# Optimization experiments

Measured on AMD Instinct MI355X. Metric: run time of the kernel, lower is better.

Reference implementation:

```python
import jax, jax.numpy as jnp
import numpy as np

N, E, F_IN, H, G, C = 50000, 800000, 128, 128, 64, 10
EPS = 1e-5


def _glorot_lin(key, fin, fout):
    s = 1.0 / np.sqrt(fin)
    return jax.random.uniform(key, (fin, fout), jnp.float32, -s, s)


def setup_inputs() -> dict:
    key = jax.random.key(0)
    ks = jax.random.split(key, 24)
    x = jax.random.normal(ks[0], (N, F_IN), jnp.float32)
    edge_index = jax.random.randint(ks[1], (2, E), 0, N)
    batch = jnp.sort(jax.random.randint(ks[2], (N,), 0, G))
    inp = {"x": x, "edge_index": edge_index, "batch": batch}
    # GCNConv weights [in, out] and biases
    dims = [(F_IN, H), (H, H), (H, H), (H, H)]
    for i, (fi, fo) in enumerate(dims, start=1):
        inp[f"W{i}"] = _glorot_lin(ks[2 + i], fi, fo)
        inp[f"b{i}"] = jnp.zeros((fo,), jnp.float32)
    # BatchNorm affine params
    for i in range(1, 4):
        inp[f"g{i}"] = jnp.ones((H,), jnp.float32)
        inp[f"be{i}"] = jnp.zeros((H,), jnp.float32)
    # MLP head
    inp["lw1"] = _glorot_lin(ks[10], 2 * H, H)
    inp["lb1"] = jnp.zeros((H,), jnp.float32)
    inp["lw2"] = _glorot_lin(ks[11], H, C)
    inp["lb2"] = jnp.zeros((C,), jnp.float32)
    return inp


def _gcn_conv(h_in, W, b, src, dst, norm_e, self_norm):
    # linear transform then symmetric-normalized aggregation (incl. self loops)
    h = h_in @ W                                            # [N, out]
    agg = jax.ops.segment_sum(h[src] * norm_e[:, None], dst, num_segments=N)
    return agg + h * self_norm[:, None] + b


def _batch_norm(x, gamma, beta):
    mu = jnp.mean(x, axis=0)
    var = jnp.var(x, axis=0)
    return (x - mu) * jax.lax.rsqrt(var + EPS) * gamma + beta


def reference(x, edge_index, batch, W1, b1, W2, b2, W3, b3, W4, b4,
              g1, be1, g2, be2, g3, be3, lw1, lb1, lw2, lb2):
    src, dst = edge_index[0], edge_index[1]
    # degrees with self loops; GCN symmetric normalization
    deg = jax.ops.segment_sum(jnp.ones((E,), jnp.float32), dst, num_segments=N) + 1.0
    dinv = jax.lax.rsqrt(deg)
    norm_e = dinv[src] * dinv[dst]   # per-edge norm
    self_norm = 1.0 / deg            # self-loop norm = dinv*dinv

    h = jax.nn.relu(_batch_norm(_gcn_conv(x, W1, b1, src, dst, norm_e, self_norm), g1, be1))
    h = jax.nn.relu(_batch_norm(_gcn_conv(h, W2, b2, src, dst, norm_e, self_norm), g2, be2))
    h = jax.nn.relu(_batch_norm(_gcn_conv(h, W3, b3, src, dst, norm_e, self_norm), g3, be3))
    h = jax.nn.relu(_gcn_conv(h, W4, b4, src, dst, norm_e, self_norm))

    counts = jax.ops.segment_sum(jnp.ones((N,), jnp.float32), batch, num_segments=G)
    x_mean = jax.ops.segment_sum(h, batch, num_segments=G) / counts[:, None]
    x_max = jax.ops.segment_max(h, batch, num_segments=G)
    z = jnp.concatenate([x_mean, x_max], axis=1)            # [G, 2H]

    z = jax.nn.relu(z @ lw1 + lb1)
    # dropout is identity in eval mode
    return z @ lw2 + lb2                                    # [G, C]
```

## Files before the change

kernel.cpp:

```cpp
#include <hip/hip_runtime.h>

#define N_NODES 50000
#define N_EDGES 800000
#define HID     128
#define NGRAPH  64
#define BN_EPS  1e-5f
#define SCAN_B  98

__global__ __launch_bounds__(256) void degbounds_kernel(const int* __restrict__ ei,
                                                        int* __restrict__ degi,
                                                        const int* __restrict__ batch,
                                                        int* __restrict__ bound) {
    const int i = blockIdx.x * 256 + threadIdx.x;
    if (i < N_EDGES) atomicAdd(&degi[ei[N_EDGES + i]], 1);
    if (i < N_NODES) {
        const int b = batch[i];
        if (i == 0) {
            for (int g = 0; g <= b; ++g) bound[g] = 0;
        } else {
            const int pb = batch[i - 1];
            for (int g = pb + 1; g <= b; ++g) bound[g] = i;
        }
        if (i == N_NODES - 1) {
            for (int g = b + 1; g <= NGRAPH; ++g) bound[g] = N_NODES;
        }
    }
}

__global__ __launch_bounds__(512) void scan1_kernel(const int* __restrict__ degi,
                                                    int* __restrict__ row_start,
                                                    int* __restrict__ partials,
                                                    float* __restrict__ dinv) {
    __shared__ int sh[512];
    const int t = threadIdx.x;
    const int i = blockIdx.x * 512 + t;
    const int v = (i < N_NODES) ? degi[i] : 0;
    if (i < N_NODES) dinv[i] = rsqrtf((float)v + 1.0f);
    sh[t] = v;
    __syncthreads();
#pragma unroll
    for (int off = 1; off < 512; off <<= 1) {
        const int add = (t >= off) ? sh[t - off] : 0;
        __syncthreads();
        sh[t] += add;
        __syncthreads();
    }
    if (i < N_NODES) row_start[i] = sh[t] - v;
    if (t == 511) partials[blockIdx.x] = sh[511];
}

__global__ __launch_bounds__(128) void scan2_kernel(int* __restrict__ partials,
                                                    int* __restrict__ row_start) {
    __shared__ int sh[SCAN_B + 1];
    const int t = threadIdx.x;
    if (t < SCAN_B) sh[t] = partials[t];
    __syncthreads();
    if (t == 0) {
        int run = 0;
        for (int b = 0; b < SCAN_B; ++b) { const int v = sh[b]; sh[b] = run; run += v; }
        sh[SCAN_B] = run;
    }
    __syncthreads();
    if (t < SCAN_B) partials[t] = sh[t];
    if (t == 0) row_start[N_NODES] = sh[SCAN_B];
}

__global__ __launch_bounds__(512) void scan3_kernel(int* __restrict__ row_start,
                                                    const int* __restrict__ partials) {
    const int i = blockIdx.x * 512 + threadIdx.x;
    if (i < N_NODES) row_start[i] += partials[blockIdx.x];
}

__global__ __launch_bounds__(256) void scatter_kernel(const int* __restrict__ ei,
                                                      const float* __restrict__ dinv,
                                                      const int* __restrict__ row_start,
                                                      int* __restrict__ cursor,
                                                      float2* __restrict__ csr_sw) {
    int e = blockIdx.x * 256 + threadIdx.x;
    if (e >= N_EDGES) return;
    const int src = ei[e];
    const int dst = ei[N_EDGES + e];
    const int pos = row_start[dst] + atomicAdd(&cursor[dst], 1);
    float2 sw;
    sw.x = __int_as_float(src);
    sw.y = dinv[src] * dinv[dst];
    csr_sw[pos] = sw;
}

__global__ __launch_bounds__(256) void gemm_kernel(const float* __restrict__ X,
                                                   const float* __restrict__ W,
                                                   const float* __restrict__ stats,
                                                   const float* __restrict__ gamma,
                                                   const float* __restrict__ beta,
                                                   const int use_bn,
                                                   float* __restrict__ hout) {
    __shared__ float xs[64][128];
    __shared__ float wsm[32][128];
    __shared__ float scs[128], shs[128];
    const int tid = threadIdx.x;
    const int block_row = blockIdx.x * 64;

    if (use_bn && tid < 128) {
        const float invN = 1.0f / (float)N_NODES;
        const float mu = stats[tid] * invN;
        const float var = stats[128 + tid] * invN - mu * mu;
        const float sc = rsqrtf(var + BN_EPS) * gamma[tid];
        scs[tid] = sc;
        shs[tid] = fmaf(-mu, sc, beta[tid]);
    }
    if (use_bn) __syncthreads();

    {
        const float4* Xv = (const float4*)(X + (size_t)block_row * HID);
        float4* xsv = (float4*)&xs[0][0];
        int rows_valid = N_NODES - block_row;
        if (rows_valid > 64) rows_valid = 64;
        const int max4 = rows_valid * 32;
        for (int i = tid; i < 64 * 32; i += 256) {
            float4 v = (i < max4) ? Xv[i] : make_float4(0.f, 0.f, 0.f, 0.f);
            if (use_bn) {
                const int c4 = (i & 31) * 4;
                const float4 sc = *(const float4*)&scs[c4];
                const float4 sh = *(const float4*)&shs[c4];
                v.x = fmaxf(fmaf(v.x, sc.x, sh.x), 0.f);
                v.y = fmaxf(fmaf(v.y, sc.y, sh.y), 0.f);
                v.z = fmaxf(fmaf(v.z, sc.z, sh.z), 0.f);
                v.w = fmaxf(fmaf(v.w, sc.w, sh.w), 0.f);
            }
            xsv[i] = v;
        }
    }

    const int cg = (tid & 31) * 4;
    const int r0 = (tid >> 5) * 8;

    float acc[8][4];
#pragma unroll
    for (int r = 0; r < 8; ++r)
#pragma unroll
        for (int j = 0; j < 4; ++j) acc[r][j] = 0.f;

    for (int kc = 0; kc < 4; ++kc) {
        __syncthreads();
        {
            const float4* Wv = (const float4*)(W + kc * 32 * HID);
            float4* wsv = (float4*)&wsm[0][0];
            for (int i = tid; i < 32 * 32; i += 256) wsv[i] = Wv[i];
        }
        __syncthreads();
#pragma unroll
        for (int kk = 0; kk < 32; ++kk) {
            const float4 w4 = *(const float4*)(&wsm[kk][cg]);
            const int k = kc * 32 + kk;
#pragma unroll
            for (int r = 0; r < 8; ++r) {
                const float xv = xs[r0 + r][k];
                acc[r][0] = fmaf(xv, w4.x, acc[r][0]);
                acc[r][1] = fmaf(xv, w4.y, acc[r][1]);
                acc[r][2] = fmaf(xv, w4.z, acc[r][2]);
                acc[r][3] = fmaf(xv, w4.w, acc[r][3]);
            }
        }
    }

#pragma unroll
    for (int r = 0; r < 8; ++r) {
        const int row = block_row + r0 + r;
        if (row < N_NODES)
            *(float4*)(hout + (size_t)row * HID + cg) =
                make_float4(acc[r][0], acc[r][1], acc[r][2], acc[r][3]);
    }
}

__global__ __launch_bounds__(256) void agg_csr_kernel(const int* __restrict__ row_start,
                                                      const float2* __restrict__ csr_sw,
                                                      const float* __restrict__ h,
                                                      const float* __restrict__ dinv,
                                                      const float* __restrict__ bias,
                                                      float* __restrict__ agg) {
    const int node = blockIdx.x * 4 + (threadIdx.x >> 6);
    if (node >= N_NODES) return;
    const int lane = threadIdx.x & 63;
    const int c = lane * 2;
    const int beg = row_start[node];
    const int end = row_start[node + 1];

    const float dv = dinv[node];
    const float sn = dv * dv;
    const float2 hv = *(const float2*)(h + (size_t)node * HID + c);
    const float2 bv = *(const float2*)(bias + c);
    float2 a0 = make_float2(fmaf(hv.x, sn, bv.x), fmaf(hv.y, sn, bv.y));
    float2 a1 = make_float2(0.f, 0.f), a2 = make_float2(0.f, 0.f),
           a3 = make_float2(0.f, 0.f), a4 = make_float2(0.f, 0.f),
           a5 = make_float2(0.f, 0.f), a6 = make_float2(0.f, 0.f),
           a7 = make_float2(0.f, 0.f);

    int p = beg;
    for (; p + 8 <= end; p += 8) {
        const float2 e0 = csr_sw[p];
        const float2 e1 = csr_sw[p + 1];
        const float2 e2 = csr_sw[p + 2];
        const float2 e3 = csr_sw[p + 3];
        const float2 e4 = csr_sw[p + 4];
        const float2 e5 = csr_sw[p + 5];
        const float2 e6 = csr_sw[p + 6];
        const float2 e7 = csr_sw[p + 7];
        const float2 v0 = *(const float2*)(h + (size_t)__float_as_int(e0.x) * HID + c);
        const float2 v1 = *(const float2*)(h + (size_t)__float_as_int(e1.x) * HID + c);
        const float2 v2 = *(const float2*)(h + (size_t)__float_as_int(e2.x) * HID + c);
        const float2 v3 = *(const float2*)(h + (size_t)__float_as_int(e3.x) * HID + c);
        const float2 v4 = *(const float2*)(h + (size_t)__float_as_int(e4.x) * HID + c);
        const float2 v5 = *(const float2*)(h + (size_t)__float_as_int(e5.x) * HID + c);
        const float2 v6 = *(const float2*)(h + (size_t)__float_as_int(e6.x) * HID + c);
        const float2 v7 = *(const float2*)(h + (size_t)__float_as_int(e7.x) * HID + c);
        a0.x = fmaf(v0.x, e0.y, a0.x); a0.y = fmaf(v0.y, e0.y, a0.y);
        a1.x = fmaf(v1.x, e1.y, a1.x); a1.y = fmaf(v1.y, e1.y, a1.y);
        a2.x = fmaf(v2.x, e2.y, a2.x); a2.y = fmaf(v2.y, e2.y, a2.y);
        a3.x = fmaf(v3.x, e3.y, a3.x); a3.y = fmaf(v3.y, e3.y, a3.y);
        a4.x = fmaf(v4.x, e4.y, a4.x); a4.y = fmaf(v4.y, e4.y, a4.y);
        a5.x = fmaf(v5.x, e5.y, a5.x); a5.y = fmaf(v5.y, e5.y, a5.y);
        a6.x = fmaf(v6.x, e6.y, a6.x); a6.y = fmaf(v6.y, e6.y, a6.y);
        a7.x = fmaf(v7.x, e7.y, a7.x); a7.y = fmaf(v7.y, e7.y, a7.y);
    }
    for (; p + 4 <= end; p += 4) {
        const float2 e0 = csr_sw[p];
        const float2 e1 = csr_sw[p + 1];
        const float2 e2 = csr_sw[p + 2];
        const float2 e3 = csr_sw[p + 3];
        const float2 v0 = *(const float2*)(h + (size_t)__float_as_int(e0.x) * HID + c);
        const float2 v1 = *(const float2*)(h + (size_t)__float_as_int(e1.x) * HID + c);
        const float2 v2 = *(const float2*)(h + (size_t)__float_as_int(e2.x) * HID + c);
        const float2 v3 = *(const float2*)(h + (size_t)__float_as_int(e3.x) * HID + c);
        a0.x = fmaf(v0.x, e0.y, a0.x); a0.y = fmaf(v0.y, e0.y, a0.y);
        a1.x = fmaf(v1.x, e1.y, a1.x); a1.y = fmaf(v1.y, e1.y, a1.y);
        a2.x = fmaf(v2.x, e2.y, a2.x); a2.y = fmaf(v2.y, e2.y, a2.y);
        a3.x = fmaf(v3.x, e3.y, a3.x); a3.y = fmaf(v3.y, e3.y, a3.y);
    }
    for (; p < end; ++p) {
        const float2 e0 = csr_sw[p];
        const float2 v0 = *(const float2*)(h + (size_t)__float_as_int(e0.x) * HID + c);
        a0.x = fmaf(v0.x, e0.y, a0.x); a0.y = fmaf(v0.y, e0.y, a0.y);
    }
    a0.x += (a1.x + a2.x) + (a3.x + a4.x) + (a5.x + a6.x) + a7.x;
    a0.y += (a1.y + a2.y) + (a3.y + a4.y) + (a5.y + a6.y) + a7.y;
    *(float2*)(agg + (size_t)node * HID + c) = a0;
}

__global__ __launch_bounds__(256) void bn_stats_kernel(const float* __restrict__ a,
                                                       float* __restrict__ stats) {
    const int c = threadIdx.x & 127;
    const int half = threadIdx.x >> 7;
    const int row0 = blockIdx.x * 128;
    int rend = row0 + 128;
    if (rend > N_NODES) rend = N_NODES;
    float s = 0.f, sq = 0.f;
    for (int r = row0 + half; r < rend; r += 2) {
        const float v = a[(size_t)r * HID + c];
        s += v;
        sq = fmaf(v, v, sq);
    }
    __shared__ float sh[2][2][128];
    sh[0][half][c] = s;
    sh[1][half][c] = sq;
    __syncthreads();
    if (half == 0) {
        atomicAdd(&stats[c], sh[0][0][c] + sh[0][1][c]);
        atomicAdd(&stats[HID + c], sh[1][0][c] + sh[1][1][c]);
    }
}

__global__ __launch_bounds__(256) void pool_seg_kernel(const float* __restrict__ a,
                                                       const int* __restrict__ bound,
                                                       float* __restrict__ z) {
    const int g = blockIdx.x;
    const int cl = threadIdx.x & 31;
    const int c = blockIdx.y * 32 + cl;
    const int par = threadIdx.x >> 5;
    const int beg = bound[g], end = bound[g + 1];
    float s = 0.f, m = 0.f;
    for (int r = beg + par; r < end; r += 8) {
        const float v = fmaxf(a[(size_t)r * HID + c], 0.f);
        s += v;
        m = fmaxf(m, v);
    }
    __shared__ float ssum[8][32];
    __shared__ float smax[8][32];
    ssum[par][cl] = s;
    smax[par][cl] = m;
    __syncthreads();
    if (par == 0) {
        float ts = 0.f, tm = 0.f;
#pragma unroll
        for (int p = 0; p < 8; ++p) { ts += ssum[p][cl]; tm = fmaxf(tm, smax[p][cl]); }
        const float cntf = (float)(end - beg);
        z[g * 256 + c] = ts / fmaxf(cntf, 1.f);
        z[g * 256 + 128 + c] = tm;
    }
}

__global__ __launch_bounds__(128) void head_kernel(const float* __restrict__ z,
                                                   const float* __restrict__ lw1,
                                                   const float* __restrict__ lb1,
                                                   const float* __restrict__ lw2,
                                                   const float* __restrict__ lb2,
                                                   float* __restrict__ out) {
    __shared__ float zin[256];
    __shared__ float z1[128];
    const int g = blockIdx.x;
    const int t = threadIdx.x;
    zin[t] = z[g * 256 + t];
    zin[128 + t] = z[g * 256 + 128 + t];
    __syncthreads();
    float accv = lb1[t];
#pragma unroll 4
    for (int k = 0; k < 256; ++k) accv = fmaf(zin[k], lw1[k * 128 + t], accv);
    z1[t] = fmaxf(accv, 0.f);
    __syncthreads();
    if (t < 10) {
        float o = lb2[t];
#pragma unroll 4
        for (int k = 0; k < 128; ++k) o = fmaf(z1[k], lw2[k * 10 + t], o);
        out[g * 10 + t] = o;
    }
}

extern "C" void kernel_launch(void* const* d_in, const int* in_sizes, int n_in,
                              void* d_out, int out_size, void* d_ws, size_t ws_size,
                              hipStream_t stream) {
    const float* x     = (const float*)d_in[0];
    const int*   ei    = (const int*)d_in[1];
    const int*   batch = (const int*)d_in[2];
    const float* W[4]  = {(const float*)d_in[3], (const float*)d_in[5],
                          (const float*)d_in[7], (const float*)d_in[9]};
    const float* B[4]  = {(const float*)d_in[4], (const float*)d_in[6],
                          (const float*)d_in[8], (const float*)d_in[10]};
    const float* Gm[3] = {(const float*)d_in[11], (const float*)d_in[13],
                          (const float*)d_in[15]};
    const float* Be[3] = {(const float*)d_in[12], (const float*)d_in[14],
                          (const float*)d_in[16]};
    const float* lw1 = (const float*)d_in[17];
    const float* lb1 = (const float*)d_in[18];
    const float* lw2 = (const float*)d_in[19];
    const float* lb2 = (const float*)d_in[20];

    char* ws = (char*)d_ws;
    float*  dinv      = (float*)ws;
    float*  stats     = (float*)(ws + 50000u * 4);
    float*  z         = (float*)(ws + 50256u * 4);
    int*    degi      = (int*)  (ws + 66640u * 4);
    int*    cursor    = (int*)  (ws + 116640u * 4);
    int*    row_start = (int*)  (ws + 166640u * 4);
    int*    bound     = (int*)  (ws + 216644u * 4);
    float2* csr_sw    = (float2*)(ws + 216712u * 4);
    float*  hbuf      = (float*)(ws + 1816712u * 4);
    float*  abuf      = (float*)(ws + 8216712u * 4);
    int*    partials  = (int*)  (ws + 14616712u * 4);

    hipMemsetAsync(degi, 0, 100000u * sizeof(int), stream);
    degbounds_kernel<<<(N_EDGES + 255) / 256, 256, 0, stream>>>(ei, degi, batch, bound);
    scan1_kernel<<<SCAN_B, 512, 0, stream>>>(degi, row_start, partials, dinv);
    scan2_kernel<<<1, 128, 0, stream>>>(partials, row_start);
    scan3_kernel<<<SCAN_B, 512, 0, stream>>>(row_start, partials);
    scatter_kernel<<<(N_EDGES + 255) / 256, 256, 0, stream>>>(ei, dinv, row_start,
                                                              cursor, csr_sw);

    const float* cur = x;
    for (int l = 0; l < 4; ++l) {
        gemm_kernel<<<(N_NODES + 63) / 64, 256, 0, stream>>>(
            cur, W[l], stats, l > 0 ? Gm[l - 1] : Gm[0], l > 0 ? Be[l - 1] : Be[0],
            l > 0 ? 1 : 0, hbuf);
        agg_csr_kernel<<<(N_NODES + 3) / 4, 256, 0, stream>>>(row_start, csr_sw, hbuf,
                                                              dinv, B[l], abuf);
        if (l < 3) {
            hipMemsetAsync(stats, 0, 256 * sizeof(float), stream);
            bn_stats_kernel<<<(N_NODES + 127) / 128, 256, 0, stream>>>(abuf, stats);
        }
        cur = abuf;
    }

    pool_seg_kernel<<<dim3(NGRAPH, 4), 256, 0, stream>>>(abuf, bound, z);
    head_kernel<<<NGRAPH, 128, 0, stream>>>(z, lw1, lb1, lw2, lb2, (float*)d_out);
}
```

Baseline: 742.8 us.

## Fuse BN statistics into CSR aggregation and retile GEMM with swizzled shared memory

The separate bn_stats kernel and its per-layer memset are removed. The aggregation kernel becomes a grid-stride loop over a fixed 2048-block grid that accumulates per-channel sum and sum-of-squares and atomically adds them into a per-layer stats slice, which is zeroed once up front. This avoids re-reading the 25.6 MB activation buffer three times and cuts launches. The GEMM is retiled to 4 rows by 8 columns per thread with an XOR-swizzled X tile and float4 X reads, reducing LDS bank conflicts and LDS traffic per FMA. The fixed grid may lower occupancy balance for the gather.

```diff
diff --git a/kernel.cpp b/kernel.cpp
--- a/kernel.cpp
+++ b/kernel.cpp
@@ -6,6 +6,7 @@
 #define NGRAPH  64
 #define BN_EPS  1e-5f
 #define SCAN_B  98
+#define AGG_GRID 2048
 
 __global__ __launch_bounds__(256) void degbounds_kernel(const int* __restrict__ ei,
                                                         int* __restrict__ degi,
@@ -111,15 +112,15 @@
     if (use_bn) __syncthreads();
 
     {
-        const float4* Xv = (const float4*)(X + (size_t)block_row * HID);
-        float4* xsv = (float4*)&xs[0][0];
         int rows_valid = N_NODES - block_row;
         if (rows_valid > 64) rows_valid = 64;
-        const int max4 = rows_valid * 32;
         for (int i = tid; i < 64 * 32; i += 256) {
-            float4 v = (i < max4) ? Xv[i] : make_float4(0.f, 0.f, 0.f, 0.f);
+            const int r = i >> 5;
+            const int c4 = (i & 31) * 4;
+            float4 v = make_float4(0.f, 0.f, 0.f, 0.f);
+            if (r < rows_valid)
+                v = *(const float4*)(X + (size_t)(block_row + r) * HID + c4);
             if (use_bn) {
-                const int c4 = (i & 31) * 4;
                 const float4 sc = *(const float4*)&scs[c4];
                 const float4 sh = *(const float4*)&shs[c4];
                 v.x = fmaxf(fmaf(v.x, sc.x, sh.x), 0.f);
@@ -127,18 +128,19 @@
                 v.z = fmaxf(fmaf(v.z, sc.z, sh.z), 0.f);
                 v.w = fmaxf(fmaf(v.w, sc.w, sh.w), 0.f);
             }
-            xsv[i] = v;
-        }
-    }
-
-    const int cg = (tid & 31) * 4;
-    const int r0 = (tid >> 5) * 8;
-
-    float acc[8][4];
-#pragma unroll
-    for (int r = 0; r < 8; ++r)
-#pragma unroll
-        for (int j = 0; j < 4; ++j) acc[r][j] = 0.f;
+            *(float4*)&xs[r][c4 ^ (((r >> 2) & 3) << 2)] = v;
+        }
+    }
+
+    const int cgA = (tid & 15) * 4;
+    const int r0 = (tid >> 4) * 4;
+    const int kswz = ((r0 >> 2) & 3) << 2;
+
+    float acc[4][8];
+#pragma unroll
+    for (int r = 0; r < 4; ++r)
+#pragma unroll
+        for (int j = 0; j < 8; ++j) acc[r][j] = 0.f;
 
     for (int kc = 0; kc < 4; ++kc) {
         __syncthreads();
@@ -149,26 +151,41 @@
         }
         __syncthreads();
 #pragma unroll
-        for (int kk = 0; kk < 32; ++kk) {
-            const float4 w4 = *(const float4*)(&wsm[kk][cg]);
-            const int k = kc * 32 + kk;
-#pragma unroll
-            for (int r = 0; r < 8; ++r) {
-                const float xv = xs[r0 + r][k];
-                acc[r][0] = fmaf(xv, w4.x, acc[r][0]);
-                acc[r][1] = fmaf(xv, w4.y, acc[r][1]);
-                acc[r][2] = fmaf(xv, w4.z, acc[r][2]);
-                acc[r][3] = fmaf(xv, w4.w, acc[r][3]);
+        for (int kk4 = 0; kk4 < 32; kk4 += 4) {
+            float4 xv[4];
+#pragma unroll
+            for (int j = 0; j < 4; ++j)
+                xv[j] = *(const float4*)&xs[r0 + j][(kc * 32 + kk4) ^ kswz];
+#pragma unroll
+            for (int dk = 0; dk < 4; ++dk) {
+                const float4 wa = *(const float4*)&wsm[kk4 + dk][cgA];
+                const float4 wb = *(const float4*)&wsm[kk4 + dk][cgA + 64];
+#pragma unroll
+                for (int r = 0; r < 4; ++r) {
+                    const float xvv = ((const float*)&xv[r])[dk];
+                    acc[r][0] = fmaf(xvv, wa.x, acc[r][0]);
+                    acc[r][1] = fmaf(xvv, wa.y, acc[r][1]);
+                    acc[r][2] = fmaf(xvv, wa.z, acc[r][2]);
+                    acc[r][3] = fmaf(xvv, wa.w, acc[r][3]);
+                    acc[r][4] = fmaf(xvv, wb.x, acc[r][4]);
+                    acc[r][5] = fmaf(xvv, wb.y, acc[r][5]);
+                    acc[r][6] = fmaf(xvv, wb.z, acc[r][6]);
+                    acc[r][7] = fmaf(xvv, wb.w, acc[r][7]);
+                }
             }
         }
     }
 
 #pragma unroll
-    for (int r = 0; r < 8; ++r) {
+    for (int r = 0; r < 4; ++r) {
         const int row = block_row + r0 + r;
-        if (row < N_NODES)
-            *(float4*)(hout + (size_t)row * HID + cg) =
+        if (row < N_NODES) {
+            float* hp = hout + (size_t)row * HID;
+            *(float4*)(hp + cgA) =
                 make_float4(acc[r][0], acc[r][1], acc[r][2], acc[r][3]);
+            *(float4*)(hp + cgA + 64) =
+                make_float4(acc[r][4], acc[r][5], acc[r][6], acc[r][7]);
+        }
     }
 }
 
@@ -177,95 +194,99 @@
                                                       const float* __restrict__ h,
                                                       const float* __restrict__ dinv,
                                                       const float* __restrict__ bias,
-                                                      float* __restrict__ agg) {
-    const int node = blockIdx.x * 4 + (threadIdx.x >> 6);
-    if (node >= N_NODES) return;
+                                                      float* __restrict__ agg,
+                                                      float* __restrict__ stats_out,
+                                                      const int do_stats) {
     const int lane = threadIdx.x & 63;
+    const int wv = threadIdx.x >> 6;
     const int c = lane * 2;
-    const int beg = row_start[node];
-    const int end = row_start[node + 1];
-
-    const float dv = dinv[node];
-    const float sn = dv * dv;
-    const float2 hv = *(const float2*)(h + (size_t)node * HID + c);
     const float2 bv = *(const float2*)(bias + c);
-    float2 a0 = make_float2(fmaf(hv.x, sn, bv.x), fmaf(hv.y, sn, bv.y));
-    float2 a1 = make_float2(0.f, 0.f), a2 = make_float2(0.f, 0.f),
-           a3 = make_float2(0.f, 0.f), a4 = make_float2(0.f, 0.f),
-           a5 = make_float2(0.f, 0.f), a6 = make_float2(0.f, 0.f),
-           a7 = make_float2(0.f, 0.f);
-
-    int p = beg;
-    for (; p + 8 <= end; p += 8) {
-        const float2 e0 = csr_sw[p];
-        const float2 e1 = csr_sw[p + 1];
-        const float2 e2 = csr_sw[p + 2];
-        const float2 e3 = csr_sw[p + 3];
-        const float2 e4 = csr_sw[p + 4];
-        const float2 e5 = csr_sw[p + 5];
-        const float2 e6 = csr_sw[p + 6];
-        const float2 e7 = csr_sw[p + 7];
-        const float2 v0 = *(const float2*)(h + (size_t)__float_as_int(e0.x) * HID + c);
-        const float2 v1 = *(const float2*)(h + (size_t)__float_as_int(e1.x) * HID + c);
-        const float2 v2 = *(const float2*)(h + (size_t)__float_as_int(e2.x) * HID + c);
-        const float2 v3 = *(const float2*)(h + (size_t)__float_as_int(e3.x) * HID + c);
-        const float2 v4 = *(const float2*)(h + (size_t)__float_as_int(e4.x) * HID + c);
-        const float2 v5 = *(const float2*)(h + (size_t)__float_as_int(e5.x) * HID + c);
-        const float2 v6 = *(const float2*)(h + (size_t)__float_as_int(e6.x) * HID + c);
-        const float2 v7 = *(const float2*)(h + (size_t)__float_as_int(e7.x) * HID + c);
-        a0.x = fmaf(v0.x, e0.y, a0.x); a0.y = fmaf(v0.y, e0.y, a0.y);
-        a1.x = fmaf(v1.x, e1.y, a1.x); a1.y = fmaf(v1.y, e1.y, a1.y);
-        a2.x = fmaf(v2.x, e2.y, a2.x); a2.y = fmaf(v2.y, e2.y, a2.y);
-        a3.x = fmaf(v3.x, e3.y, a3.x); a3.y = fmaf(v3.y, e3.y, a3.y);
-        a4.x = fmaf(v4.x, e4.y, a4.x); a4.y = fmaf(v4.y, e4.y, a4.y);
-        a5.x = fmaf(v5.x, e5.y, a5.x); a5.y = fmaf(v5.y, e5.y, a5.y);
-        a6.x = fmaf(v6.x, e6.y, a6.x); a6.y = fmaf(v6.y, e6.y, a6.y);
-        a7.x = fmaf(v7.x, e7.y, a7.x); a7.y = fmaf(v7.y, e7.y, a7.y);
-    }
-    for (; p + 4 <= end; p += 4) {
-        const float2 e0 = csr_sw[p];
-        const float2 e1 = csr_sw[p + 1];
-        const float2 e2 = csr_sw[p + 2];
-        const float2 e3 = csr_sw[p + 3];
-        const float2 v0 = *(const float2*)(h + (size_t)__float_as_int(e0.x) * HID + c);
-        const float2 v1 = *(const float2*)(h + (size_t)__float_as_int(e1.x) * HID + c);
-        const float2 v2 = *(const float2*)(h + (size_t)__float_as_int(e2.x) * HID + c);
-        const float2 v3 = *(const float2*)(h + (size_t)__float_as_int(e3.x) * HID + c);
-        a0.x = fmaf(v0.x, e0.y, a0.x); a0.y = fmaf(v0.y, e0.y, a0.y);
-        a1.x = fmaf(v1.x, e1.y, a1.x); a1.y = fmaf(v1.y, e1.y, a1.y);
-        a2.x = fmaf(v2.x, e2.y, a2.x); a2.y = fmaf(v2.y, e2.y, a2.y);
-        a3.x = fmaf(v3.x, e3.y, a3.x); a3.y = fmaf(v3.y, e3.y, a3.y);
-    }
-    for (; p < end; ++p) {
-        const float2 e0 = csr_sw[p];
-        const float2 v0 = *(const float2*)(h + (size_t)__float_as_int(e0.x) * HID + c);
-        a0.x = fmaf(v0.x, e0.y, a0.x); a0.y = fmaf(v0.y, e0.y, a0.y);
-    }
-    a0.x += (a1.x + a2.x) + (a3.x + a4.x) + (a5.x + a6.x) + a7.x;
-    a0.y += (a1.y + a2.y) + (a3.y + a4.y) + (a5.y + a6.y) + a7.y;
-    *(float2*)(agg + (size_t)node * HID + c) = a0;
-}
-
-__global__ __launch_bounds__(256) void bn_stats_kernel(const float* __restrict__ a,
-                                                       float* __restrict__ stats) {
-    const int c = threadIdx.x & 127;
-    const int half = threadIdx.x >> 7;
-    const int row0 = blockIdx.x * 128;
-    int rend = row0 + 128;
-    if (rend > N_NODES) rend = N_NODES;
-    float s = 0.f, sq = 0.f;
-    for (int r = row0 + half; r < rend; r += 2) {
-        const float v = a[(size_t)r * HID + c];
-        s += v;
-        sq = fmaf(v, v, sq);
-    }
-    __shared__ float sh[2][2][128];
-    sh[0][half][c] = s;
-    sh[1][half][c] = sq;
-    __syncthreads();
-    if (half == 0) {
-        atomicAdd(&stats[c], sh[0][0][c] + sh[0][1][c]);
-        atomicAdd(&stats[HID + c], sh[1][0][c] + sh[1][1][c]);
+
+    float2 ssum = make_float2(0.f, 0.f);
+    float2 ssq  = make_float2(0.f, 0.f);
+
+    for (int base = blockIdx.x * 4; base < N_NODES; base += AGG_GRID * 4) {
+        const int node = base + wv;
+        if (node >= N_NODES) continue;
+        const int beg = row_start[node];
+        const int end = row_start[node + 1];
+
+        const float dv = dinv[node];
+        const float sn = dv * dv;
+        const float2 hv = *(const float2*)(h + (size_t)node * HID + c);
+        float2 a0 = make_float2(fmaf(hv.x, sn, bv.x), fmaf(hv.y, sn, bv.y));
+        float2 a1 = make_float2(0.f, 0.f), a2 = make_float2(0.f, 0.f),
+               a3 = make_float2(0.f, 0.f), a4 = make_float2(0.f, 0.f),
+               a5 = make_float2(0.f, 0.f), a6 = make_float2(0.f, 0.f),
+               a7 = make_float2(0.f, 0.f);
+
+        int p = beg;
+        for (; p + 8 <= end; p += 8) {
+            const float2 e0 = csr_sw[p];
+            const float2 e1 = csr_sw[p + 1];
+            const float2 e2 = csr_sw[p + 2];
+            const float2 e3 = csr_sw[p + 3];
+            const float2 e4 = csr_sw[p + 4];
+            const float2 e5 = csr_sw[p + 5];
+            const float2 e6 = csr_sw[p + 6];
+            const float2 e7 = csr_sw[p + 7];
+            const float2 v0 = *(const float2*)(h + (size_t)__float_as_int(e0.x) * HID + c);
+            const float2 v1 = *(const float2*)(h + (size_t)__float_as_int(e1.x) * HID + c);
+            const float2 v2 = *(const float2*)(h + (size_t)__float_as_int(e2.x) * HID + c);
+            const float2 v3 = *(const float2*)(h + (size_t)__float_as_int(e3.x) * HID + c);
+            const float2 v4 = *(const float2*)(h + (size_t)__float_as_int(e4.x) * HID + c);
+            const float2 v5 = *(const float2*)(h + (size_t)__float_as_int(e5.x) * HID + c);
+            const float2 v6 = *(const float2*)(h + (size_t)__float_as_int(e6.x) * HID + c);
+            const float2 v7 = *(const float2*)(h + (size_t)__float_as_int(e7.x) * HID + c);
+            a0.x = fmaf(v0.x, e0.y, a0.x); a0.y = fmaf(v0.y, e0.y, a0.y);
+            a1.x = fmaf(v1.x, e1.y, a1.x); a1.y = fmaf(v1.y, e1.y, a1.y);
+            a2.x = fmaf(v2.x, e2.y, a2.x); a2.y = fmaf(v2.y, e2.y, a2.y);
+            a3.x = fmaf(v3.x, e3.y, a3.x); a3.y = fmaf(v3.y, e3.y, a3.y);
+            a4.x = fmaf(v4.x, e4.y, a4.x); a4.y = fmaf(v4.y, e4.y, a4.y);
+            a5.x = fmaf(v5.x, e5.y, a5.x); a5.y = fmaf(v5.y, e5.y, a5.y);
+            a6.x = fmaf(v6.x, e6.y, a6.x); a6.y = fmaf(v6.y, e6.y, a6.y);
+            a7.x = fmaf(v7.x, e7.y, a7.x); a7.y = fmaf(v7.y, e7.y, a7.y);
+        }
+        for (; p + 4 <= end; p += 4) {
+            const float2 e0 = csr_sw[p];
+            const float2 e1 = csr_sw[p + 1];
+            const float2 e2 = csr_sw[p + 2];
+            const float2 e3 = csr_sw[p + 3];
+            const float2 v0 = *(const float2*)(h + (size_t)__float_as_int(e0.x) * HID + c);
+            const float2 v1 = *(const float2*)(h + (size_t)__float_as_int(e1.x) * HID + c);
+            const float2 v2 = *(const float2*)(h + (size_t)__float_as_int(e2.x) * HID + c);
+            const float2 v3 = *(const float2*)(h + (size_t)__float_as_int(e3.x) * HID + c);
+            a0.x = fmaf(v0.x, e0.y, a0.x); a0.y = fmaf(v0.y, e0.y, a0.y);
+            a1.x = fmaf(v1.x, e1.y, a1.x); a1.y = fmaf(v1.y, e1.y, a1.y);
+            a2.x = fmaf(v2.x, e2.y, a2.x); a2.y = fmaf(v2.y, e2.y, a2.y);
+            a3.x = fmaf(v3.x, e3.y, a3.x); a3.y = fmaf(v3.y, e3.y, a3.y);
+        }
+        for (; p < end; ++p) {
+            const float2 e0 = csr_sw[p];
+            const float2 v0 = *(const float2*)(h + (size_t)__float_as_int(e0.x) * HID + c);
+            a0.x = fmaf(v0.x, e0.y, a0.x); a0.y = fmaf(v0.y, e0.y, a0.y);
+        }
+        a0.x += (a1.x + a2.x) + (a3.x + a4.x) + (a5.x + a6.x) + a7.x;
+        a0.y += (a1.y + a2.y) + (a3.y + a4.y) + (a5.y + a6.y) + a7.y;
+        *(float2*)(agg + (size_t)node * HID + c) = a0;
+
+        ssum.x += a0.x; ssum.y += a0.y;
+        ssq.x = fmaf(a0.x, a0.x, ssq.x); ssq.y = fmaf(a0.y, a0.y, ssq.y);
+    }
+
+    if (do_stats) {
+        __shared__ float s1[4][128];
+        __shared__ float s2[4][128];
+        s1[wv][c] = ssum.x; s1[wv][c + 1] = ssum.y;
+        s2[wv][c] = ssq.x;  s2[wv][c + 1] = ssq.y;
+        __syncthreads();
+        const int t = threadIdx.x;
+        if (t < 128) {
+            atomicAdd(&stats_out[t], s1[0][t] + s1[1][t] + s1[2][t] + s1[3][t]);
+        } else {
+            const int c2 = t - 128;
+            atomicAdd(&stats_out[128 + c2], s2[0][c2] + s2[1][c2] + s2[2][c2] + s2[3][c2]);
+        }
     }
 }
 
@@ -345,18 +366,19 @@
 
     char* ws = (char*)d_ws;
     float*  dinv      = (float*)ws;
-    float*  stats     = (float*)(ws + 50000u * 4);
-    float*  z         = (float*)(ws + 50256u * 4);
-    int*    degi      = (int*)  (ws + 66640u * 4);
-    int*    cursor    = (int*)  (ws + 116640u * 4);
-    int*    row_start = (int*)  (ws + 166640u * 4);
-    int*    bound     = (int*)  (ws + 216644u * 4);
-    float2* csr_sw    = (float2*)(ws + 216712u * 4);
-    float*  hbuf      = (float*)(ws + 1816712u * 4);
-    float*  abuf      = (float*)(ws + 8216712u * 4);
-    int*    partials  = (int*)  (ws + 14616712u * 4);
+    float*  stats3    = (float*)(ws + 50000u * 4);
+    float*  z         = (float*)(ws + 50768u * 4);
+    int*    degi      = (int*)  (ws + 67152u * 4);
+    int*    cursor    = (int*)  (ws + 117152u * 4);
+    int*    row_start = (int*)  (ws + 167152u * 4);
+    int*    bound     = (int*)  (ws + 217156u * 4);
+    float2* csr_sw    = (float2*)(ws + 217224u * 4);
+    float*  hbuf      = (float*)(ws + 1817224u * 4);
+    float*  abuf      = (float*)(ws + 8217224u * 4);
+    int*    partials  = (int*)  (ws + 14617224u * 4);
 
     hipMemsetAsync(degi, 0, 100000u * sizeof(int), stream);
+    hipMemsetAsync(stats3, 0, 768u * sizeof(float), stream);
     degbounds_kernel<<<(N_EDGES + 255) / 256, 256, 0, stream>>>(ei, degi, batch, bound);
     scan1_kernel<<<SCAN_B, 512, 0, stream>>>(degi, row_start, partials, dinv);
     scan2_kernel<<<1, 128, 0, stream>>>(partials, row_start);
@@ -367,14 +389,12 @@
     const float* cur = x;
     for (int l = 0; l < 4; ++l) {
         gemm_kernel<<<(N_NODES + 63) / 64, 256, 0, stream>>>(
-            cur, W[l], stats, l > 0 ? Gm[l - 1] : Gm[0], l > 0 ? Be[l - 1] : Be[0],
+            cur, W[l], l > 0 ? stats3 + (l - 1) * 256 : stats3,
+            l > 0 ? Gm[l - 1] : Gm[0], l > 0 ? Be[l - 1] : Be[0],
             l > 0 ? 1 : 0, hbuf);
-        agg_csr_kernel<<<(N_NODES + 3) / 4, 256, 0, stream>>>(row_start, csr_sw, hbuf,
-                                                              dinv, B[l], abuf);
-        if (l < 3) {
-            hipMemsetAsync(stats, 0, 256 * sizeof(float), stream);
-            bn_stats_kernel<<<(N_NODES + 127) / 128, 256, 0, stream>>>(abuf, stats);
-        }
+        agg_csr_kernel<<<AGG_GRID, 256, 0, stream>>>(
+            row_start, csr_sw, hbuf, dinv, B[l], abuf,
+            l < 3 ? stats3 + l * 256 : stats3, l < 3 ? 1 : 0);
         cur = abuf;
     }
 
```

Result: no change. 756.4 us (+1.8%).
